# Performance work log

Hardware: AMD Instinct MI355X
Metric: run time of the kernel (lower is better)

## Reference

```python
import jax, jax.numpy as jnp
import numpy as np

DIM = 512
HEADS = 8
HEAD_DIM = 64
INNER = HEADS * HEAD_DIM  # 512
FF = DIM * 2
EPS = 1e-5


def layernorm(x, g, b):
    mu = jnp.mean(x, axis=-1, keepdims=True)
    var = jnp.var(x, axis=-1, keepdims=True)
    return (x - mu) * jax.lax.rsqrt(var + EPS) * g + b


def setup_inputs() -> dict:
    key = jax.random.key(0)
    ks = jax.random.split(key, 10)
    s = lambda fan_in: 1.0 / np.sqrt(fan_in)
    return {
        "x": jax.random.normal(ks[0], (4, 2048, DIM), dtype=jnp.float32),
        "ln1_g": jnp.ones((DIM,), jnp.float32),
        "ln1_b": jnp.zeros((DIM,), jnp.float32),
        "w_qkv": jax.random.normal(ks[1], (DIM, 3 * INNER), jnp.float32) * s(DIM),
        "w_out": jax.random.normal(ks[2], (INNER, DIM), jnp.float32) * s(INNER),
        "b_out": jnp.zeros((DIM,), jnp.float32),
        "ln2_g": jnp.ones((DIM,), jnp.float32),
        "ln2_b": jnp.zeros((DIM,), jnp.float32),
        "w1": jax.random.normal(ks[3], (DIM, FF), jnp.float32) * s(DIM),
        "b1": jnp.zeros((FF,), jnp.float32),
        "w2": jax.random.normal(ks[4], (FF, DIM), jnp.float32) * s(FF),
        "b2": jnp.zeros((DIM,), jnp.float32),
    }


def reference(x, ln1_g, ln1_b, w_qkv, w_out, b_out, ln2_g, ln2_b, w1, b1, w2, b2):
    b, n, _ = x.shape
    # --- pre-LN MHSA ---
    h = layernorm(x, ln1_g, ln1_b)
    qkv = h @ w_qkv  # [b, n, 3*inner]
    q, k, v = jnp.split(qkv, 3, axis=-1)
    to_heads = lambda t: t.reshape(b, n, HEADS, HEAD_DIM).transpose(0, 2, 1, 3)
    q, k, v = to_heads(q), to_heads(k), to_heads(v)
    scores = jnp.einsum('bhid,bhjd->bhij', q, k) * (HEAD_DIM ** -0.5)
    attn = jax.nn.softmax(scores, axis=-1)
    attended = jnp.einsum('bhij,bhjd->bhid', attn, v)
    attended = attended.transpose(0, 2, 1, 3).reshape(b, n, INNER)
    x = attended @ w_out + b_out + x
    # --- pre-LN MLP ---
    h = layernorm(x, ln2_g, ln2_b)
    h = jax.nn.gelu(h @ w1 + b1, approximate=False)
    x = h @ w2 + b2 + x
    return x
```

## Files before the change

### kernel.cpp

```cpp
#include <hip/hip_runtime.h>
#include <math.h>


#define TOKENS 8192
#define SEQ    2048
typedef unsigned short u16;
typedef __attribute__((ext_vector_type(8))) _Float16 h8;
typedef __attribute__((ext_vector_type(4))) float f32x4;
typedef __attribute__((ext_vector_type(4))) unsigned short u16x4;

#define BAR_V0 asm volatile("s_waitcnt vmcnt(0) lgkmcnt(0)\n\ts_barrier" ::: "memory")

__device__ __forceinline__ u16 f2h(float f) {
    _Float16 h = (_Float16)f;
    return __builtin_bit_cast(u16, h);
}
__device__ __forceinline__ void a16(void* lds, const void* g) {
    __builtin_amdgcn_global_load_lds(
        (const __attribute__((address_space(1))) unsigned int*)g,
        (__attribute__((address_space(3))) unsigned int*)lds, 16, 0, 0);
}
__device__ __forceinline__ float gelu_exact(float v) {
    return 0.5f * v * (1.0f + erff(v * 0.70710678118654752f));
}

__global__ __launch_bounds__(256) void prep_k(const float* __restrict__ wqkv,
                                              const float* __restrict__ wout,
                                              const float* __restrict__ w1,
                                              const float* __restrict__ w2,
                                              u16* __restrict__ dqkv,
                                              u16* __restrict__ dout,
                                              u16* __restrict__ d1,
                                              u16* __restrict__ d2,
                                              const float* __restrict__ x,
                                              const float* __restrict__ g,
                                              const float* __restrict__ bta,
                                              u16* __restrict__ oh) {
    const int tid = threadIdx.x;
    if (blockIdx.x >= 512) {
        const int lane = tid & 63;
        const int row  = ((blockIdx.x - 512) << 2) + (tid >> 6);
        const float* xr = x + ((size_t)row << 9) + (lane << 3);
        float v[8];
        *(float4*)&v[0] = *(const float4*)xr;
        *(float4*)&v[4] = *(const float4*)(xr + 4);
        float s = 0.f, ss = 0.f;
#pragma unroll
        for (int i = 0; i < 8; i++) { s += v[i]; ss += v[i] * v[i]; }
#pragma unroll
        for (int m = 32; m; m >>= 1) {
            s  += __shfl_xor(s, m, 64);
            ss += __shfl_xor(ss, m, 64);
        }
        const float mu   = s * (1.0f / 512.0f);
        const float rstd = rsqrtf(ss * (1.0f / 512.0f) - mu * mu + 1e-5f);
        float gg[8], bb[8];
        *(float4*)&gg[0] = *(const float4*)(g + (lane << 3));
        *(float4*)&gg[4] = *(const float4*)(g + (lane << 3) + 4);
        *(float4*)&bb[0] = *(const float4*)(bta + (lane << 3));
        *(float4*)&bb[4] = *(const float4*)(bta + (lane << 3) + 4);
        union { u16 us[8]; uint4 q; } H;
#pragma unroll
        for (int i = 0; i < 8; i++) H.us[i] = f2h((v[i] - mu) * rstd * gg[i] + bb[i]);
        *(uint4*)&oh[((size_t)row << 9) + (lane << 3)] = H.q;
        return;
    }
    __shared__ float t[64][65];
    int b = blockIdx.x;
    const float* src; u16* dst; int K, N, n0, k0;
    if (b < 192)      { src = wqkv; dst = dqkv; K = 512;  N = 1536; n0 = (b % 24) << 6; k0 = (b / 24) << 6; }
    else if (b < 256) { b -= 192; src = wout; dst = dout; K = 512;  N = 512;  n0 = (b & 7) << 6;  k0 = (b >> 3) << 6; }
    else if (b < 384) { b -= 256; src = w1;   dst = d1;   K = 512;  N = 1024; n0 = (b & 15) << 6; k0 = (b >> 4) << 6; }
    else              { b -= 384; src = w2;   dst = d2;   K = 1024; N = 512;  n0 = (b & 7) << 6;  k0 = (b >> 3) << 6; }
    {
        const int kr = tid >> 2, nc = (tid & 3) << 4;
        const float* p = src + (size_t)(k0 + kr) * N + n0 + nc;
#pragma unroll
        for (int i = 0; i < 4; i++)
            *(float4*)&t[kr][nc + (i << 2)] = *(const float4*)(p + (i << 2));
    }
    __syncthreads();
    {
        const int nr = tid >> 2, kc = (tid & 3) << 4;
        union { u16 us[16]; uint4 q[2]; } H;
#pragma unroll
        for (int i = 0; i < 16; i++) H.us[i] = f2h(t[kc + i][nr]);
        const size_t o = (size_t)(n0 + nr) * K + k0 + kc;
        *(uint4*)&dst[o] = H.q[0];
        *(uint4*)&dst[o + 8] = H.q[1];
    }
}

__global__ __launch_bounds__(256) void ln_k(const float* __restrict__ x,
                                            const float* __restrict__ g,
                                            const float* __restrict__ bta,
                                            u16* __restrict__ oh) {
    const int lane = threadIdx.x & 63;
    const int row  = (blockIdx.x << 2) + (threadIdx.x >> 6);
    const float* xr = x + ((size_t)row << 9) + (lane << 3);
    float v[8];
    *(float4*)&v[0] = *(const float4*)xr;
    *(float4*)&v[4] = *(const float4*)(xr + 4);
    float s = 0.f, ss = 0.f;
#pragma unroll
    for (int i = 0; i < 8; i++) { s += v[i]; ss += v[i] * v[i]; }
#pragma unroll
    for (int m = 32; m; m >>= 1) {
        s  += __shfl_xor(s, m, 64);
        ss += __shfl_xor(ss, m, 64);
    }
    const float mu   = s * (1.0f / 512.0f);
    const float rstd = rsqrtf(ss * (1.0f / 512.0f) - mu * mu + 1e-5f);
    float gg[8], bb[8];
    *(float4*)&gg[0] = *(const float4*)(g + (lane << 3));
    *(float4*)&gg[4] = *(const float4*)(g + (lane << 3) + 4);
    *(float4*)&bb[0] = *(const float4*)(bta + (lane << 3));
    *(float4*)&bb[4] = *(const float4*)(bta + (lane << 3) + 4);
    union { u16 us[8]; uint4 q; } H;
#pragma unroll
    for (int i = 0; i < 8; i++) H.us[i] = f2h((v[i] - mu) * rstd * gg[i] + bb[i]);
    *(uint4*)&oh[((size_t)row << 9) + (lane << 3)] = H.q;
}

template <int EPI>
__global__ __launch_bounds__(256, 3) void sgemm_k(
    const u16* __restrict__ A, const u16* __restrict__ B,
    const float* __restrict__ bias, const float* __restrict__ res,
    float* __restrict__ Cf, u16* __restrict__ Ch, u16* __restrict__ Dh,
    int M, int N, int K) {
    __shared__ u16 sm[16384];
    const int tid = threadIdx.x;
    const int lane = tid & 63, wv = tid >> 6;
    const int col = lane & 15, quad = lane >> 4;
    const int wm = (wv & 1) << 6, wn = (wv >> 1) << 6;
    const int bm = blockIdx.y << 7, bn = blockIdx.x << 7;

    const int r0 = tid >> 2,         c0 = (tid & 3) ^ ((r0 >> 1) & 3);
    const int r1 = (tid + 256) >> 2, c1 = (tid & 3) ^ ((r1 >> 1) & 3);
    const u16* Ag0 = A + (size_t)(bm + r0) * K + c0 * 8;
    const u16* Ag1 = A + (size_t)(bm + r1) * K + c1 * 8;
    const u16* Bg0 = B + (size_t)(bn + r0) * K + c0 * 8;
    const u16* Bg1 = B + (size_t)(bn + r1) * K + c1 * 8;
    const int lw0 = wv * 512, lw1 = wv * 512 + 2048;
    const int swz = (col >> 1) & 3;
    const f32x4 z4 = {0.f, 0.f, 0.f, 0.f};
    f32x4 acc[4][4] = {{z4,z4,z4,z4},{z4,z4,z4,z4},{z4,z4,z4,z4},{z4,z4,z4,z4}};

    a16(&sm[lw0],        Ag0);  a16(&sm[lw1],        Ag1);
    a16(&sm[lw0 + 4096], Bg0);  a16(&sm[lw1 + 4096], Bg1);

    int ib = 0;
    for (int k0 = 0; k0 < K; k0 += 32, ib ^= 1) {
        BAR_V0;
        if (k0 + 32 < K) {
            const int nb = (ib ^ 1) * 8192;
            const int kn = k0 + 32;
            a16(&sm[nb + lw0],        Ag0 + kn);  a16(&sm[nb + lw1],        Ag1 + kn);
            a16(&sm[nb + lw0 + 4096], Bg0 + kn);  a16(&sm[nb + lw1 + 4096], Bg1 + kn);
        }
        const int cb = ib * 8192;
        h8 af[4];
#pragma unroll
        for (int mt = 0; mt < 4; mt++) {
            const int ra = cb + (wm + (mt << 4) + col) * 32 + ((quad ^ swz) << 3);
            af[mt] = *(const h8*)&sm[ra];
        }
#pragma unroll
        for (int nt = 0; nt < 4; nt++) {
            const int rb = cb + 4096 + (wn + (nt << 4) + col) * 32 + ((quad ^ swz) << 3);
            h8 bf = *(const h8*)&sm[rb];
#pragma unroll
            for (int mt = 0; mt < 4; mt++)
                acc[mt][nt] = __builtin_amdgcn_mfma_f32_16x16x32_f16(af[mt], bf, acc[mt][nt], 0, 0, 0);
        }
    }

    if constexpr (EPI == 0) {
        if (bn >= 1024) {
            const int hd0  = (bn - 1024) >> 6;
            const int b8   = (bm >> 11) << 3;
            const int keyb = bm & 2047;
            __syncthreads();
#pragma unroll
            for (int hf = 0; hf < 2; hf++) {
                if ((wv >> 1) == hf) {
#pragma unroll
                    for (int mt = 0; mt < 4; mt++)
#pragma unroll
                    for (int rr = 0; rr < 4; rr++) {
                        const int key = wm + (mt << 4) + (quad << 2) + rr;
#pragma unroll
                        for (int nt = 0; nt < 4; nt++) {
                            const int dl = (nt << 4) + col;
                            sm[dl * 136 + key] = f2h(acc[mt][nt][rr]);
                        }
                    }
                }
                __syncthreads();
                {
                    const int d = tid >> 2;
#pragma unroll
                    for (int c = 0; c < 4; c++) {
                        const int key0 = ((((tid & 3) << 2) + c) << 3);
                        const size_t gb = ((size_t)(b8 + hd0 + hf) << 17)
                                        + ((size_t)d << 11) + keyb + key0;
                        *(uint4*)&Dh[gb] = *(const uint4*)&sm[d * 136 + key0];
                    }
                }
                __syncthreads();
            }
            return;
        }
    }

    float bs[4];
    if constexpr (EPI >= 1) {
#pragma unroll
        for (int nt = 0; nt < 4; nt++) bs[nt] = bias[bn + wn + (nt << 4) + col];
    }
#pragma unroll
    for (int mt = 0; mt < 4; mt++) {
#pragma unroll
        for (int rr = 0; rr < 4; rr++) {
            const int row = bm + wm + (mt << 4) + (quad << 2) + rr;
#pragma unroll
            for (int nt = 0; nt < 4; nt++) {
                const int colg = bn + wn + (nt << 4) + col;
                float v = acc[mt][nt][rr];
                if constexpr (EPI == 0) {
                    const int b = row >> 11, key = row & 2047;
                    if (bn < 512) {
                        Cf[((size_t)row << 9) + colg] = v;
                    } else {
                        const int hd = (colg - 512) >> 6, d = colg & 63;
                        Ch[((size_t)((b << 3) + hd) << 17) + (key << 6) + d] = f2h(v);
                    }
                } else if constexpr (EPI == 2) {
                    Ch[(size_t)row * N + colg] = f2h(gelu_exact(v + bs[nt]));
                } else {
                    const size_t o = (size_t)row * N + colg;
                    Cf[o] = v + bs[nt] + res[o];
                }
            }
        }
    }
}

__global__ __launch_bounds__(256, 4) void attn_k(const float* __restrict__ q,
                                                 const u16* __restrict__ kh,
                                                 const u16* __restrict__ vth,
                                                 u16* __restrict__ ah) {
    __shared__ u16 sm[20480];
    const int tid = threadIdx.x;
    const int lane = tid & 63, wv = tid >> 6;
    const int col = lane & 15, quad = lane >> 4;
    const int qt = blockIdx.x, bh = blockIdx.y;
    const int b = bh >> 3, h = bh & 7;
    const size_t tok0 = (size_t)b * SEQ;
    const size_t bhK = (size_t)bh << 17;
    const int q0 = qt << 6;

    h8 qf[2];
    {
        const int qrow = q0 + (wv << 4) + col;
        const float* qp = q + ((tok0 + qrow) << 9) + (h << 6) + (quad << 3);
#pragma unroll
        for (int kc = 0; kc < 2; kc++) {
            float v[8];
            *(float4*)&v[0] = *(const float4*)(qp + (kc << 5));
            *(float4*)&v[4] = *(const float4*)(qp + (kc << 5) + 4);
            union { u16 us[8]; h8 v8; } H;
#pragma unroll
            for (int i = 0; i < 8; i++) H.us[i] = f2h(v[i] * 0.125f);
            qf[kc] = H.v8;
        }
    }

    const f32x4 z4 = {0.f, 0.f, 0.f, 0.f};
    f32x4 o[4] = {z4, z4, z4, z4};
    float m_run = -1e30f, l_run = 0.f;

    size_t kbz[2], vbz[2];
    int doff[2];
#pragma unroll
    for (int j = 0; j < 2; j++) {
        const int C = (((j << 2) + wv) << 6) + lane;
        const int sr = C >> 3, sp = (C & 7) ^ (sr & 7);
        kbz[j] = bhK + ((size_t)sr << 6) + (sp << 3);
        vbz[j] = bhK + ((size_t)sr << 11) + (sp << 3);
        doff[j] = (((j << 2) + wv) << 9);
    }

#pragma unroll
    for (int j = 0; j < 2; j++) a16(&sm[doff[j]], kh + kbz[j]);
#pragma unroll
    for (int j = 0; j < 2; j++) a16(&sm[8192 + doff[j]], vth + vbz[j]);
#pragma unroll
    for (int j = 0; j < 2; j++) a16(&sm[4096 + doff[j]], kh + kbz[j] + 4096);

    int ib = 0;
    for (int jt = 0; jt < 32; jt++, ib ^= 1) {
        if (jt < 31) {
            asm volatile("s_waitcnt vmcnt(2) lgkmcnt(0)\n\ts_barrier" ::: "memory");
        } else {
            asm volatile("s_waitcnt vmcnt(0) lgkmcnt(0)\n\ts_barrier" ::: "memory");
        }
        if (jt < 31) {
            const size_t vo = (size_t)(jt + 1) << 6;
            const int vb = 8192 + ((ib ^ 1) << 12);
#pragma unroll
            for (int j = 0; j < 2; j++) a16(&sm[vb + doff[j]], vth + vbz[j] + vo);
        }

        const int cb = ib << 12;
        f32x4 st[4] = {z4, z4, z4, z4};
        __builtin_amdgcn_s_setprio(1);
#pragma unroll
        for (int kb = 0; kb < 4; kb++) {
            const int key = (kb << 4) + col;
            const int r64 = key << 6, k7 = key & 7;
#pragma unroll
            for (int kc = 0; kc < 2; kc++) {
                const int ofs = cb + r64 + ((((kc << 2) + quad) ^ k7) << 3);
                h8 kf = *(const h8*)&sm[ofs];
                st[kb] = __builtin_amdgcn_mfma_f32_16x16x32_f16(kf, qf[kc], st[kb], 0, 0, 0);
            }
        }
        __builtin_amdgcn_s_setprio(0);

        float mx = st[0][0];
#pragma unroll
        for (int kb = 0; kb < 4; kb++)
#pragma unroll
            for (int r = 0; r < 4; r++) mx = fmaxf(mx, st[kb][r]);
        mx = fmaxf(mx, __shfl_xor(mx, 16));
        mx = fmaxf(mx, __shfl_xor(mx, 32));
        const float mn = fmaxf(m_run, mx);
        const float alp = __expf(m_run - mn);
        m_run = mn;
        float p[16];
        float rs = 0.0f;
#pragma unroll
        for (int kb = 0; kb < 4; kb++)
#pragma unroll
            for (int r = 0; r < 4; r++) {
                float e = __expf(st[kb][r] - mn);
                p[(kb << 2) + r] = e;
                rs += e;
            }
        rs += __shfl_xor(rs, 16);
        rs += __shfl_xor(rs, 32);
        l_run = l_run * alp + rs;
        float aO[4];
#pragma unroll
        for (int r = 0; r < 4; r++) aO[r] = __shfl(alp, (quad << 2) + r);
#pragma unroll
        for (int db = 0; db < 4; db++) {
            o[db][0] *= aO[0]; o[db][1] *= aO[1];
            o[db][2] *= aO[2]; o[db][3] *= aO[3];
        }
        const int prow = (wv << 4) + col;
        const int p64 = prow << 6, p7 = prow & 7;
#pragma unroll
        for (int kb = 0; kb < 4; kb++) {
            u16x4 hv;
#pragma unroll
            for (int r = 0; r < 4; r++) hv[r] = f2h(p[(kb << 2) + r]);
            const int c = (kb << 1) + (quad >> 1);
            *(u16x4*)&sm[16384 + p64 + ((c ^ p7) << 3) + ((quad & 1) << 2)] = hv;
        }

        asm volatile("s_waitcnt lgkmcnt(0)\n\ts_barrier" ::: "memory");

        if (jt < 30) {
            const size_t ko = (size_t)(jt + 2) << 12;
            const int kb2 = ib << 12;
#pragma unroll
            for (int j = 0; j < 2; j++) a16(&sm[kb2 + doff[j]], kh + kbz[j] + ko);
        }

        h8 pf[2];
#pragma unroll
        for (int kc = 0; kc < 2; kc++)
            pf[kc] = *(const h8*)&sm[16384 + p64 + ((((kc << 2) + quad) ^ p7) << 3)];

        const int vbase = 8192 + (ib << 12);
        __builtin_amdgcn_s_setprio(1);
#pragma unroll
        for (int db = 0; db < 4; db++) {
            const int d = (db << 4) + col;
            const int v64 = vbase + (d << 6), d7 = d & 7;
#pragma unroll
            for (int kc = 0; kc < 2; kc++) {
                h8 vf = *(const h8*)&sm[v64 + ((((kc << 2) + quad) ^ d7) << 3)];
                o[db] = __builtin_amdgcn_mfma_f32_16x16x32_f16(pf[kc], vf, o[db], 0, 0, 0);
            }
        }
        __builtin_amdgcn_s_setprio(0);
    }

    float linv[4];
#pragma unroll
    for (int r = 0; r < 4; r++) linv[r] = 1.0f / __shfl(l_run, (quad << 2) + r);
#pragma unroll
    for (int r = 0; r < 4; r++) {
        const size_t rowo = ((tok0 + q0 + (wv << 4) + (quad << 2) + r) << 9)
                            + (h << 6) + col;
#pragma unroll
        for (int db = 0; db < 4; db++)
            ah[rowo + (db << 4)] = f2h(o[db][r] * linv[r]);
    }
}

extern "C" void kernel_launch(void* const* d_in, const int* in_sizes, int n_in,
                              void* d_out, int out_size, void* d_ws, size_t ws_size,
                              hipStream_t stream) {
    const float* x     = (const float*)d_in[0];
    const float* ln1_g = (const float*)d_in[1];
    const float* ln1_b = (const float*)d_in[2];
    const float* w_qkv = (const float*)d_in[3];
    const float* w_out = (const float*)d_in[4];
    const float* b_out = (const float*)d_in[5];
    const float* ln2_g = (const float*)d_in[6];
    const float* ln2_b = (const float*)d_in[7];
    const float* w1    = (const float*)d_in[8];
    const float* b1    = (const float*)d_in[9];
    const float* w2    = (const float*)d_in[10];
    const float* b2    = (const float*)d_in[11];
    float* out = (float*)d_out;

    u16* wqkvh = (u16*)d_ws;
    u16* wouth = wqkvh + 1536 * 512;
    u16* w1h   = wouth + 512 * 512;
    u16* w2h   = w1h + 1024 * 512;
    u16* hbuf  = w2h + 512 * 1024;
    float* qbuf = (float*)(hbuf + (size_t)TOKENS * 512);
    float* x2   = qbuf;
    u16* kh  = (u16*)(qbuf + (size_t)TOKENS * 512);
    u16* vth = kh + (size_t)32 * 131072;
    u16* gh  = kh;

    prep_k<<<2560, 256, 0, stream>>>(w_qkv, w_out, w1, w2, wqkvh, wouth, w1h, w2h,
                                     x, ln1_g, ln1_b, hbuf);
    sgemm_k<0><<<dim3(12, 64), 256, 0, stream>>>(hbuf, wqkvh, nullptr, nullptr,
                                                 qbuf, kh, vth, TOKENS, 1536, 512);
    attn_k<<<dim3(32, 32), 256, 0, stream>>>(qbuf, kh, vth, hbuf);
    sgemm_k<1><<<dim3(4, 64), 256, 0, stream>>>(hbuf, wouth, b_out, x,
                                                x2, nullptr, nullptr, TOKENS, 512, 512);
    ln_k<<<TOKENS / 4, 256, 0, stream>>>(x2, ln2_g, ln2_b, hbuf);
    sgemm_k<2><<<dim3(8, 64), 256, 0, stream>>>(hbuf, w1h, b1, nullptr,
                                                nullptr, gh, nullptr, TOKENS, 1024, 512);
    sgemm_k<3><<<dim3(4, 64), 256, 0, stream>>>(gh, w2h, b2, x2,
                                                out, nullptr, nullptr, TOKENS, 512, 1024);
}
```

Baseline: 249.4 us.

## Triple-buffer K tiles, drop mid-iteration barrier, lazy softmax rescale with exp2

The attention kernel moves K from a double to a triple LDS buffer, so the prefetch for tile jt+2 can be issued at the top of the loop. This removes the second block-wide barrier per iteration, leaving only a local lgkmcnt wait before the P reads, which is sound because each wave reads only its own P rows. The softmax switches to exp2 by folding log2(e) into the Q scale, and it skips rescaling the running max and output unless some row's max grows by more than 11. P is packed to fp16 with cvt_pkrtz. LDS use grows, so the occupancy hint drops from 4 to 3 blocks per CU, and the lazy rescale lets unnormalised exponentials grow up to 2^11 in fp16 P.

```diff
diff --git a/kernel.cpp b/kernel.cpp
--- a/kernel.cpp
+++ b/kernel.cpp
@@ -14,6 +14,9 @@
 __device__ __forceinline__ u16 f2h(float f) {
     _Float16 h = (_Float16)f;
     return __builtin_bit_cast(u16, h);
+}
+__device__ __forceinline__ unsigned int pk2h(float a, float b) {
+    return __builtin_bit_cast(unsigned int, __builtin_amdgcn_cvt_pkrtz(a, b));
 }
 __device__ __forceinline__ void a16(void* lds, const void* g) {
     __builtin_amdgcn_global_load_lds(
@@ -246,11 +249,11 @@
     }
 }
 
-__global__ __launch_bounds__(256, 4) void attn_k(const float* __restrict__ q,
+__global__ __launch_bounds__(256, 3) void attn_k(const float* __restrict__ q,
                                                  const u16* __restrict__ kh,
                                                  const u16* __restrict__ vth,
                                                  u16* __restrict__ ah) {
-    __shared__ u16 sm[20480];
+    __shared__ u16 sm[24576];
     const int tid = threadIdx.x;
     const int lane = tid & 63, wv = tid >> 6;
     const int col = lane & 15, quad = lane >> 4;
@@ -271,7 +274,7 @@
             *(float4*)&v[4] = *(const float4*)(qp + (kc << 5) + 4);
             union { u16 us[8]; h8 v8; } H;
 #pragma unroll
-            for (int i = 0; i < 8; i++) H.us[i] = f2h(v[i] * 0.125f);
+            for (int i = 0; i < 8; i++) H.us[i] = f2h(v[i] * 0.18033688011f);
             qf[kc] = H.v8;
         }
     }
@@ -294,12 +297,14 @@
 #pragma unroll
     for (int j = 0; j < 2; j++) a16(&sm[doff[j]], kh + kbz[j]);
 #pragma unroll
-    for (int j = 0; j < 2; j++) a16(&sm[8192 + doff[j]], vth + vbz[j]);
+    for (int j = 0; j < 2; j++) a16(&sm[12288 + doff[j]], vth + vbz[j]);
 #pragma unroll
     for (int j = 0; j < 2; j++) a16(&sm[4096 + doff[j]], kh + kbz[j] + 4096);
 
-    int ib = 0;
-    for (int jt = 0; jt < 32; jt++, ib ^= 1) {
+    int kcur = 0;
+    const int prow = (wv << 4) + col;
+    const int p64 = prow << 6, p7 = prow & 7;
+    for (int jt = 0; jt < 32; jt++) {
         if (jt < 31) {
             asm volatile("s_waitcnt vmcnt(2) lgkmcnt(0)\n\ts_barrier" ::: "memory");
         } else {
@@ -307,12 +312,17 @@
         }
         if (jt < 31) {
             const size_t vo = (size_t)(jt + 1) << 6;
-            const int vb = 8192 + ((ib ^ 1) << 12);
+            const int vb = 12288 + (((jt + 1) & 1) << 12);
 #pragma unroll
             for (int j = 0; j < 2; j++) a16(&sm[vb + doff[j]], vth + vbz[j] + vo);
         }
-
-        const int cb = ib << 12;
+        if (jt < 30) {
+            const size_t ko = (size_t)(jt + 2) << 12;
+            int kt = kcur + 8192; if (kt >= 12288) kt -= 12288;
+#pragma unroll
+            for (int j = 0; j < 2; j++) a16(&sm[kt + doff[j]], kh + kbz[j] + ko);
+        }
+
         f32x4 st[4] = {z4, z4, z4, z4};
         __builtin_amdgcn_s_setprio(1);
 #pragma unroll
@@ -321,7 +331,7 @@
             const int r64 = key << 6, k7 = key & 7;
 #pragma unroll
             for (int kc = 0; kc < 2; kc++) {
-                const int ofs = cb + r64 + ((((kc << 2) + quad) ^ k7) << 3);
+                const int ofs = kcur + r64 + ((((kc << 2) + quad) ^ k7) << 3);
                 h8 kf = *(const h8*)&sm[ofs];
                 st[kb] = __builtin_amdgcn_mfma_f32_16x16x32_f16(kf, qf[kc], st[kb], 0, 0, 0);
             }
@@ -335,56 +345,50 @@
             for (int r = 0; r < 4; r++) mx = fmaxf(mx, st[kb][r]);
         mx = fmaxf(mx, __shfl_xor(mx, 16));
         mx = fmaxf(mx, __shfl_xor(mx, 32));
-        const float mn = fmaxf(m_run, mx);
-        const float alp = __expf(m_run - mn);
-        m_run = mn;
+        if (__any(mx > m_run + 11.0f)) {
+            const float mn  = fmaxf(m_run, mx);
+            const float alp = exp2f(m_run - mn);
+            m_run = mn;
+            l_run *= alp;
+            float aO[4];
+#pragma unroll
+            for (int r = 0; r < 4; r++) aO[r] = __shfl(alp, (quad << 2) + r);
+#pragma unroll
+            for (int db = 0; db < 4; db++) {
+                o[db][0] *= aO[0]; o[db][1] *= aO[1];
+                o[db][2] *= aO[2]; o[db][3] *= aO[3];
+            }
+        }
         float p[16];
         float rs = 0.0f;
 #pragma unroll
         for (int kb = 0; kb < 4; kb++)
 #pragma unroll
             for (int r = 0; r < 4; r++) {
-                float e = __expf(st[kb][r] - mn);
+                float e = exp2f(st[kb][r] - m_run);
                 p[(kb << 2) + r] = e;
                 rs += e;
             }
         rs += __shfl_xor(rs, 16);
         rs += __shfl_xor(rs, 32);
-        l_run = l_run * alp + rs;
-        float aO[4];
-#pragma unroll
-        for (int r = 0; r < 4; r++) aO[r] = __shfl(alp, (quad << 2) + r);
-#pragma unroll
-        for (int db = 0; db < 4; db++) {
-            o[db][0] *= aO[0]; o[db][1] *= aO[1];
-            o[db][2] *= aO[2]; o[db][3] *= aO[3];
-        }
-        const int prow = (wv << 4) + col;
-        const int p64 = prow << 6, p7 = prow & 7;
+        l_run += rs;
 #pragma unroll
         for (int kb = 0; kb < 4; kb++) {
-            u16x4 hv;
-#pragma unroll
-            for (int r = 0; r < 4; r++) hv[r] = f2h(p[(kb << 2) + r]);
+            uint2 w;
+            w.x = pk2h(p[(kb << 2) + 0], p[(kb << 2) + 1]);
+            w.y = pk2h(p[(kb << 2) + 2], p[(kb << 2) + 3]);
             const int c = (kb << 1) + (quad >> 1);
-            *(u16x4*)&sm[16384 + p64 + ((c ^ p7) << 3) + ((quad & 1) << 2)] = hv;
-        }
-
-        asm volatile("s_waitcnt lgkmcnt(0)\n\ts_barrier" ::: "memory");
-
-        if (jt < 30) {
-            const size_t ko = (size_t)(jt + 2) << 12;
-            const int kb2 = ib << 12;
-#pragma unroll
-            for (int j = 0; j < 2; j++) a16(&sm[kb2 + doff[j]], kh + kbz[j] + ko);
-        }
+            *(uint2*)&sm[20480 + p64 + ((c ^ p7) << 3) + ((quad & 1) << 2)] = w;
+        }
+
+        asm volatile("s_waitcnt lgkmcnt(0)" ::: "memory");
 
         h8 pf[2];
 #pragma unroll
         for (int kc = 0; kc < 2; kc++)
-            pf[kc] = *(const h8*)&sm[16384 + p64 + ((((kc << 2) + quad) ^ p7) << 3)];
-
-        const int vbase = 8192 + (ib << 12);
+            pf[kc] = *(const h8*)&sm[20480 + p64 + ((((kc << 2) + quad) ^ p7) << 3)];
+
+        const int vbase = 12288 + ((jt & 1) << 12);
         __builtin_amdgcn_s_setprio(1);
 #pragma unroll
         for (int db = 0; db < 4; db++) {
@@ -397,6 +401,8 @@
             }
         }
         __builtin_amdgcn_s_setprio(0);
+
+        kcur = (kcur == 8192) ? 0 : kcur + 4096;
     }
 
     float linv[4];
```

Result: slower. 261.4 us (+4.8%).
